# Performance work log

Hardware: AMD Instinct MI355X
Metric: run time of the kernel (lower is better)

The kernel has to match this reference:

```python
import jax, jax.numpy as jnp
from jax import lax
import numpy as np

N, T, PD, TD, F, E, GB = 2048, 256, 5, 5, 128, 65536, 5


def _lstm_layer(x, Wih, Whh, bih, bhh):
    # x: [B, T, D] -> [B, T, H], torch LSTM gate order (i, f, g, o)
    B = x.shape[0]
    H = Whh.shape[1]
    b = bih + bhh

    def step(carry, xt):
        h, c = carry
        gates = xt @ Wih.T + h @ Whh.T + b
        i, f, g, o = jnp.split(gates, 4, axis=-1)
        c = jax.nn.sigmoid(f) * c + jax.nn.sigmoid(i) * jnp.tanh(g)
        h = jax.nn.sigmoid(o) * jnp.tanh(c)
        return (h, c), h

    h0 = jnp.zeros((B, H), x.dtype)
    _, hs = lax.scan(step, (h0, h0), jnp.swapaxes(x, 0, 1))
    return jnp.swapaxes(hs, 0, 1)


def _attention(x, W1, b1, W2, b2):
    # Fused prefix (cumulative causal) softmax attention.
    # Original loops over t computing softmax(scores[:, :t+1]); here:
    # ctx[t] = cumsum(e * x)[t] / cumsum(e)[t] with a global max shift
    # (softmax is shift-invariant, so this equals the per-prefix softmax).
    s = (jnp.tanh(x @ W1.T + b1) @ W2.T + b2)[..., 0]  # [B, T]
    e = jnp.exp(s - jnp.max(s, axis=1, keepdims=True))  # [B, T]
    num = jnp.cumsum(e[..., None] * x, axis=1)          # [B, T, D]
    den = jnp.cumsum(e, axis=1)[..., None]              # [B, T, 1]
    return jnp.sum(num / den, axis=1)                   # [B, D]


def _gcn(x, W, b, edge_index, edge_weight):
    # PyG GCNConv with normalize=True: add self-loops (w=1), symmetric norm.
    n = x.shape[0]
    loop = jnp.arange(n)
    row = jnp.concatenate([edge_index[0], loop])
    col = jnp.concatenate([edge_index[1], loop])
    w = jnp.concatenate([edge_weight, jnp.ones((n,), edge_weight.dtype)])
    deg = jax.ops.segment_sum(w, col, num_segments=n)
    dinv = jnp.where(deg > 0, deg ** -0.5, 0.0)
    norm = dinv[row] * w * dinv[col]
    h = x @ W.T
    out = jax.ops.segment_sum(norm[:, None] * h[row], col, num_segments=n)
    return out + b


def _forward(price, global_trend, p_weights, t_weights,
             lp_Wih0, lp_Whh0, lp_bih0, lp_bhh0, lp_Wih1, lp_Whh1, lp_bih1, lp_bhh1,
             lt_Wih0, lt_Whh0, lt_bih0, lt_bhh0, lt_Wih1, lt_Whh1, lt_bih1, lt_bhh1,
             ap_W1, ap_b1, ap_W2, ap_b2, at_W1, at_b1, at_W2, at_b2,
             gp1_W, gp1_b, gp2_W, gp2_b, gt1_W, gt1_b, gt2_W, gt2_b,
             mlp_W, mlp_b, p_edge_index, t_edge_index):
    x = _lstm_layer(price, lp_Wih0, lp_Whh0, lp_bih0, lp_bhh0)
    x = _lstm_layer(x, lp_Wih1, lp_Whh1, lp_bih1, lp_bhh1)
    x = _attention(x, ap_W1, ap_b1, ap_W2, ap_b2)            # [N, F]
    g = _lstm_layer(global_trend, lt_Wih0, lt_Whh0, lt_bih0, lt_bhh0)
    g = _lstm_layer(g, lt_Wih1, lt_Whh1, lt_bih1, lt_bhh1)
    g = _attention(g, at_W1, at_b1, at_W2, at_b2)            # [GB, F]
    pg = _gcn(x, gp1_W, gp1_b, p_edge_index, p_weights)
    pg = _gcn(pg, gp2_W, gp2_b, p_edge_index, p_weights)     # [N, F]
    # NOTE: original feeds x (not g) into the trend graph convs.
    tg = _gcn(x, gt1_W, gt1_b, t_edge_index, t_weights)
    tg = _gcn(tg, gt2_W, gt2_b, t_edge_index, t_weights)     # [N, F]
    trend = tg @ g.T                                         # [N, GB]
    feat = jnp.concatenate([pg, trend], axis=1)              # [N, F+GB]
    return jax.nn.sigmoid(feat @ mlp_W.T + mlp_b)            # [N, 1]


def setup_inputs() -> dict:
    key = jax.random.key(0)
    ks = iter(jax.random.split(key, 64))
    nrm = lambda shape, s=0.05: jax.random.normal(next(ks), shape, jnp.float32) * s
    inp = {}
    inp['price'] = jax.random.normal(next(ks), (N, T, PD), jnp.float32)
    inp['global_trend'] = jax.random.normal(next(ks), (GB, T, TD), jnp.float32)
    inp['p_edge_index'] = jax.random.randint(next(ks), (2, E), 0, N)
    inp['p_weights'] = jax.random.uniform(next(ks), (E,), jnp.float32)
    inp['t_edge_index'] = jax.random.randint(next(ks), (2, E), 0, N)
    inp['t_weights'] = jax.random.uniform(next(ks), (E,), jnp.float32)
    for pre, d in (('lp', PD), ('lt', TD)):
        inp[pre + '_Wih0'] = nrm((4 * F, d)); inp[pre + '_Whh0'] = nrm((4 * F, F))
        inp[pre + '_bih0'] = nrm((4 * F,));   inp[pre + '_bhh0'] = nrm((4 * F,))
        inp[pre + '_Wih1'] = nrm((4 * F, F)); inp[pre + '_Whh1'] = nrm((4 * F, F))
        inp[pre + '_bih1'] = nrm((4 * F,));   inp[pre + '_bhh1'] = nrm((4 * F,))
    for pre in ('ap', 'at'):
        inp[pre + '_W1'] = nrm((F, F)); inp[pre + '_b1'] = jnp.zeros((F,), jnp.float32)
        inp[pre + '_W2'] = nrm((1, F)); inp[pre + '_b2'] = jnp.zeros((1,), jnp.float32)
    for pre in ('gp', 'gt'):
        inp[pre + '1_W'] = nrm((16, F)); inp[pre + '1_b'] = jnp.zeros((16,), jnp.float32)
        inp[pre + '2_W'] = nrm((F, 16)); inp[pre + '2_b'] = jnp.zeros((F,), jnp.float32)
    inp['mlp_W'] = nrm((1, F + GB)); inp['mlp_b'] = jnp.zeros((1,), jnp.float32)
    return inp


def reference(price, global_trend, p_edge_index, p_weights, t_edge_index, t_weights,
              lp_Wih0, lp_Whh0, lp_bih0, lp_bhh0, lp_Wih1, lp_Whh1, lp_bih1, lp_bhh1,
              lt_Wih0, lt_Whh0, lt_bih0, lt_bhh0, lt_Wih1, lt_Whh1, lt_bih1, lt_bhh1,
              ap_W1, ap_b1, ap_W2, ap_b2, at_W1, at_b1, at_W2, at_b2,
              gp1_W, gp1_b, gp2_W, gp2_b, gt1_W, gt1_b, gt2_W, gt2_b,
              mlp_W, mlp_b):
    return _forward(price, global_trend, p_weights, t_weights,
                    lp_Wih0, lp_Whh0, lp_bih0, lp_bhh0, lp_Wih1, lp_Whh1, lp_bih1, lp_bhh1,
                    lt_Wih0, lt_Whh0, lt_bih0, lt_bhh0, lt_Wih1, lt_Whh1, lt_bih1, lt_bhh1,
                    ap_W1, ap_b1, ap_W2, ap_b2, at_W1, at_b1, at_W2, at_b2,
                    gp1_W, gp1_b, gp2_W, gp2_b, gt1_W, gt1_b, gt2_W, gt2_b,
                    mlp_W, mlp_b, p_edge_index, t_edge_index)
```

## Files before the change

kernel.cpp:

```cpp
#include <hip/hip_runtime.h>
#include <hip/hip_bf16.h>
#include <cstddef>

#define TT    256
#define NROW  2048
#define GBN   5
#define EDG   65536

using f32x4  = __attribute__((ext_vector_type(4))) float;
using bf16x8 = __attribute__((ext_vector_type(8))) short;

__device__ __forceinline__ void pinv(bf16x8& x) { asm volatile("" : "+v"(x)); }

__device__ __forceinline__ void barrier_lgkm() {
  asm volatile("s_waitcnt lgkmcnt(0)" ::: "memory");
  __builtin_amdgcn_s_barrier();
}

__device__ __forceinline__ float exp2fa(float x) { float r; asm("v_exp_f32 %0, %1" : "=v"(r) : "v"(x)); return r; }
__device__ __forceinline__ float rcpfa(float x)  { float r; asm("v_rcp_f32 %0, %1" : "=v"(r) : "v"(x)); return r; }
#define L2E 1.4426950408889634f
__device__ __forceinline__ float sigf(float x) { return rcpfa(1.0f + exp2fa(x * -L2E)); }
__device__ __forceinline__ float tanh_fast(float x) {
  float t = exp2fa(x * (-2.0f * L2E));
  return (1.0f - t) * rcpfa(1.0f + t);
}

enum : int {
  XBUF   = 425984,
  GBUFO  = 688128,
  DINVP  = 688768,
  DINVT  = 690816,
  H16    = 692864,
  PG1    = 725632,
// ... 51 lines not shown
    float x = (k < K1) ? Wa[(size_t)j * K1 + k] : Wb[(size_t)j * K2 + (k - K1)];
    __hip_bfloat16 hi = __float2bfloat16(x);
    ushort u;
    if (part == 0) {
      u = *(ushort*)&hi;
    } else {
      float lo = x - __bfloat162float(hi);
      __hip_bfloat16 lob = __float2bfloat16(lo);
      u = *(ushort*)&lob;
    }
    o[e] = (short)u;
  }
  ((bf16x8*)dst)[t] = o;
}

__global__ void k_zero(float* __restrict__ p, int n) {
  int i = blockIdx.x * blockDim.x + threadIdx.x;
  if (i < n) p[i] = 0.0f;
}
__global__ void k_fill1(float* __restrict__ p, int n) {
  int i = blockIdx.x * blockDim.x + threadIdx.x;
  if (i < n) p[i] = 1.0f;
}
__global__ void k_deg(const int* __restrict__ col, const float* __restrict__ w,
                      float* __restrict__ deg, int n) {
  int i = blockIdx.x * blockDim.x + threadIdx.x;
  if (i < n) atomicAdd(&deg[col[i]], w[i]);
}
__global__ void k_dinv(float* __restrict__ deg, int n) {
  int i = blockIdx.x * blockDim.x + threadIdx.x;
  if (i < n) deg[i] = rsqrtf(deg[i]);
}

__device__ static void lstm0_body(
    SmemPipe* sm, int b,
    const float* __restrict__ price, const float* __restrict__ gtrend,
    const float* __restrict__ ws_ro, ushort* __restrict__ h0W,
    const ushort* __restrict__ h0R, float* __restrict__ c0S,
    const float* __restrict__ Wih0p, const float* __restrict__ bi0p, const float* __restrict__ bh0p,
    const float* __restrict__ Wih0t, const float* __restrict__ bi0t, const float* __restrict__ bh0t,
    int t0, int TCp, int first)
{
  const int tid = threadIdx.x;
  const int w = tid >> 6, l = tid & 63;
  const int lq = l >> 4, lr = l & 15;
  const int rb = lq * 4;
  const int kcol = w * 16 + lr;
  const bool isP = b < 64;
  const int R = isP ? 32 : GBN;
  const float* seq = isP ? (price + (size_t)b * 32 * (TT * 5)) : gtrend;
  const ushort* S0 = (const ushort*)(ws_ro + (isP ? N_P0 : N_T0));
  const float* Wih0 = isP ? Wih0p : Wih0t;
  const float* bi0 = isP ? bi0p : bi0t;
  const float* bh0 = isP ? bh0p : bh0t;

  auto h0hi = sm->a;
  auto h0lo = sm->b;
  float* xsa = sm->x;

  bf16x8 wh[4][4], wl[4][4];
  #pragma unroll
  for (int kk = 0; kk < 4; ++kk)
    #pragma unroll
    for (int g = 0; g < 4; ++g) {
      int blk = (kk * 32 + (w + 8 * g)) * 2;
      wh[kk][g] = ((const bf16x8*)S0)[(blk + 0) * 64 + l];
      wl[kk][g] = ((const bf16x8*)S0)[(blk + 1) * 64 + l];
      pinv(wh[kk][g]); pinv(wl[kk][g]);
    }
  float wih0r[4][5], bg0[4];
  #pragma unroll
  for (int g = 0; g < 4; ++g) {
    int j = kcol + 128 * g;
    bg0[g] = bi0[j] + bh0[j];
    #pragma unroll
    for (int k = 0; k < 5; ++k) wih0r[g][k] = Wih0[j * 5 + k];
  }

  const size_t bstr = (size_t)b * (size_t)TCp * 8192;
  float c0[2][4] = {{0, 0, 0, 0}, {0, 0, 0, 0}};

  for (int i = tid; i < TCp * 160; i += 512) {
    int tl = i / 160, rem = i % 160, r = rem / 5, k = rem % 5;
    xsa[tl * 160 + rem] = (r < R) ? seq[(size_t)r * (TT * 5) + (size_t)(t0 + tl) * 5 + k] : 0.0f;
  }
  if (first) {
    for (int i = tid; i < 4096; i += 512) { h0hi[0][i] = 0; h0lo[0][i] = 0; }
  } else {
    const size_t lb = bstr + (size_t)(TCp - 1) * 8192;
    *(uint4*)&h0hi[0][8 * tid] = *(const uint4*)&h0R[lb + 8 * tid];
    *(uint4*)&h0lo[0][8 * tid] = *(const uint4*)&h0R[lb + 4096 + 8 * tid];
    #pragma unroll
    for (int t = 0; t < 2; ++t)
      #pragma unroll
      for (int reg = 0; reg < 4; ++reg)
        c0[t][reg] = c0S[(size_t)b * 4096 + (size_t)(t * 16 + rb + reg) * 128 + kcol];
  }
  __syncthreads();

  const int kkhi = (kcol >> 3) & 3;
  const int eo = kcol & 7;
  const int b0w = rb + 16 * kkhi;
  const int kkw = kcol >> 5;
  int wro[4];
  #pragma unroll
  for (int reg = 0; reg < 4; ++reg) wro[reg] = kkw * 512 + (b0w + (reg ^ lq)) * 8 + eo;
  const int rdo = (l ^ ((l >> 2) & 3)) * 8;

  int cur = 0;
  for (int tl = 0; tl < TCp; ++tl) {
    const int nxt = cur ^ 1;
    if (tl > 0) {
      *(uint4*)&h0W[bstr + (size_t)(tl - 1) * 8192 + 8 * tid] = *(const uint4*)&h0hi[cur][8 * tid];
      *(uint4*)&h0W[bstr + (size_t)(tl - 1) * 8192 + 4096 + 8 * tid] = *(const uint4*)&h0lo[cur][8 * tid];
    }

    f32x4 acc[2][4];
    #pragma unroll
    for (int t = 0; t < 2; ++t)
      #pragma unroll
      for (int g = 0; g < 4; ++g) acc[t][g] = (f32x4){bg0[g], bg0[g], bg0[g], bg0[g]};
    #pragma unroll
    for (int k = 0; k < 5; ++k) {
      float xv[2][4];
      #pragma unroll
      for (int t = 0; t < 2; ++t)
        #pragma unroll
        for (int reg = 0; reg < 4; ++reg)
          xv[t][reg] = xsa[tl * 160 + (t * 16 + rb + reg) * 5 + k];
      #pragma unroll
      for (int t = 0; t < 2; ++t)
        #pragma unroll
        for (int g = 0; g < 4; ++g)
          #pragma unroll
          for (int reg = 0; reg < 4; ++reg)
            acc[t][g][reg] = fmaf(xv[t][reg], wih0r[g][k], acc[t][g][reg]);
    }
    #pragma unroll
    for (int kk = 0; kk < 4; ++kk) {
      bf16x8 ah0 = *(const bf16x8*)&h0hi[cur][kk * 512 + rdo];
      bf16x8 al0 = *(const bf16x8*)&h0lo[cur][kk * 512 + rdo];
      bf16x8 ah1 = *(const bf16x8*)&h0hi[cur][2048 + kk * 512 + rdo];
      bf16x8 al1 = *(const bf16x8*)&h0lo[cur][2048 + kk * 512 + rdo];
      #pragma unroll
      for (int g = 0; g < 4; ++g) {
        acc[0][g] = __builtin_amdgcn_mfma_f32_16x16x32_bf16(ah0, wh[kk][g], acc[0][g], 0, 0, 0);
        acc[0][g] = __builtin_amdgcn_mfma_f32_16x16x32_bf16(al0, wh[kk][g], acc[0][g], 0, 0, 0);
        acc[0][g] = __builtin_amdgcn_mfma_f32_16x16x32_bf16(ah0, wl[kk][g], acc[0][g], 0, 0, 0);
        acc[1][g] = __builtin_amdgcn_mfma_f32_16x16x32_bf16(ah1, wh[kk][g], acc[1][g], 0, 0, 0);
        acc[1][g] = __builtin_amdgcn_mfma_f32_16x16x32_bf16(al1, wh[kk][g], acc[1][g], 0, 0, 0);
        acc[1][g] = __builtin_amdgcn_mfma_f32_16x16x32_bf16(ah1, wl[kk][g], acc[1][g], 0, 0, 0);
      }
    }
    #pragma unroll
    for (int t = 0; t < 2; ++t)
      #pragma unroll
      for (int reg = 0; reg < 4; ++reg) {
        float gi = acc[t][0][reg], gf = acc[t][1][reg], gg = acc[t][2][reg], go = acc[t][3][reg];
        float c = sigf(gf) * c0[t][reg] + sigf(gi) * tanh_fast(gg);
        c0[t][reg] = c;
        float h = sigf(go) * tanh_fast(c);
        __hip_bfloat16 hb = __float2bfloat16(h);
        float lo = h - __bfloat162float(hb);
        __hip_bfloat16 lb = __float2bfloat16(lo);
        h0hi[nxt][t * 2048 + wro[reg]] = *(ushort*)&hb;
        h0lo[nxt][t * 2048 + wro[reg]] = *(ushort*)&lb;
      }
    barrier_lgkm();
    cur = nxt;
  }
  *(uint4*)&h0W[bstr + (size_t)(TCp - 1) * 8192 + 8 * tid] = *(const uint4*)&h0hi[cur][8 * tid];
  *(uint4*)&h0W[bstr + (size_t)(TCp - 1) * 8192 + 4096 + 8 * tid] = *(const uint4*)&h0lo[cur][8 * tid];

  #pragma unroll
  for (int t = 0; t < 2; ++t)
    #pragma unroll
    for (int reg = 0; reg < 4; ++reg)
      c0S[(size_t)b * 4096 + (size_t)(t * 16 + rb + reg) * 128 + kcol] = c0[t][reg];
}

__device__ static void lstm1_body(
    SmemPipe* sm, int b16,
    const ushort* __restrict__ h0R, float* __restrict__ pre1, const float* __restrict__ ws_ro,
    float* __restrict__ xout, float* __restrict__ gout,
    float* __restrict__ c1S, ushort* __restrict__ h1imgS, float* __restrict__ smS,
    float* __restrict__ numS, float* __restrict__ accOS,
    const float* __restrict__ bi1p, const float* __restrict__ bh1p,
    const float* __restrict__ apB1, const float* __restrict__ apW2, const float* __restrict__ apB2,
    const float* __restrict__ bi1t, const float* __restrict__ bh1t,
    const float* __restrict__ atB1, const float* __restrict__ atW2, const float* __restrict__ atB2,
    int TCp, int first)
{
  const int tid = threadIdx.x;
  const int w = tid >> 6, l = tid & 63;
  const int lq = l >> 4, lr = l & 15;
  const int rb = lq * 4;
  const int kcol = w * 16 + lr;
  const bool isP = b16 < 128;
  const int R = isP ? 16 : GBN;
  const ushort* S1I = (const ushort*)(ws_ro + (isP ? N_P1I : N_T1I));
  const ushort* S1H = (const ushort*)(ws_ro + (isP ? N_P1H : N_T1H));
  const ushort* SA  = (const ushort*)(ws_ro + (isP ? N_PA : N_TA));
  const float* bi1 = isP ? bi1p : bi1t;
  const float* bh1 = isP ? bh1p : bh1t;
  const float* b1ap = isP ? apB1 : atB1;
  const float* w2p  = isP ? apW2 : atW2;
  const float  b2v  = isP ? apB2[0] : atB2[0];

  auto h1hi = sm->a;
  auto h1lo = sm->b;
  auto sbuf = sm->s;

  const int rdo = (l ^ ((l >> 2) & 3)) * 8;
  float* pblk = pre1 + (size_t)b16 * TCp * 8192;

  {
    const int b32 = b16 >> 1, tile = b16 & 1;
    const size_t bstr32 = (size_t)b32 * (size_t)TCp * 8192;
    float bg1[4];
    #pragma unroll
    for (int g = 0; g < 4; ++g) bg1[g] = bi1[kcol + 128 * g] + bh1[kcol + 128 * g];
    for (int g0 = 0; g0 < TCp; g0 += 2) {
      f32x4 pacc[2][4];
      #pragma unroll
      for (int ts = 0; ts < 2; ++ts)
        #pragma unroll
        for (int g = 0; g < 4; ++g) pacc[ts][g] = (f32x4){bg1[g], bg1[g], bg1[g], bg1[g]};
      #pragma unroll
      for (int kk = 0; kk < 4; ++kk) {
        bf16x8 bh_[4], bl_[4];
        #pragma unroll
        for (int g = 0; g < 4; ++g) {
          int blk = (kk * 32 + (w + 8 * g)) * 2;
          bh_[g] = ((const bf16x8*)S1I)[(blk + 0) * 64 + l];
          bl_[g] = ((const bf16x8*)S1I)[(blk + 1) * 64 + l];
        }
        #pragma unroll
        for (int ts = 0; ts < 2; ++ts) {
          const size_t tb = bstr32 + (size_t)(g0 + ts) * 8192 + tile * 2048 + kk * 512 + rdo;
          bf16x8 ah = *(const bf16x8*)&h0R[tb];
          bf16x8 al = *(const bf16x8*)&h0R[tb + 4096];
          #pragma unroll
          for (int g = 0; g < 4; ++g) {
            pacc[ts][g] = __builtin_amdgcn_mfma_f32_16x16x32_bf16(ah, bh_[g], pacc[ts][g], 0, 0, 0);
            pacc[ts][g] = __builtin_amdgcn_mfma_f32_16x16x32_bf16(al, bh_[g], pacc[ts][g], 0, 0, 0);
            pacc[ts][g] = __builtin_amdgcn_mfma_f32_16x16x32_bf16(ah, bl_[g], pacc[ts][g], 0, 0, 0);
          }
        }
      }
      #pragma unroll
      for (int ts = 0; ts < 2; ++ts)
        #pragma unroll
        for (int g = 0; g < 4; ++g)
          *(f32x4*)&pblk[(size_t)(g0 + ts) * 8192 + (size_t)tid * 16 + g * 4] = pacc[ts][g];
    }
    asm volatile("s_waitcnt vmcnt(0)" ::: "memory");
  }

  bf16x8 hh[4][4], hl[4][4];
  #pragma unroll
  for (int kk = 0; kk < 4; ++kk)
    #pragma unroll
    for (int g = 0; g < 4; ++g) {
      int blk = (kk * 32 + (w + 8 * g)) * 2;
      hh[kk][g] = ((const bf16x8*)S1H)[(blk + 0) * 64 + l];
      hl[kk][g] = ((const bf16x8*)S1H)[(blk + 1) * 64 + l];
      pinv(hh[kk][g]); pinv(hl[kk][g]);
    }
  bf16x8 wa[4], wal[4];
  #pragma unroll
  for (int kk = 0; kk < 4; ++kk) {
    wa[kk]  = ((const bf16x8*)SA)[((kk * 8 + w) * 2 + 0) * 64 + l];
    wal[kk] = ((const bf16x8*)SA)[((kk * 8 + w) * 2 + 1) * 64 + l];
    pinv(wa[kk]); pinv(wal[kk]);
  }
  const float w2r = w2p[kcol], b1ar = b1ap[kcol];

  float c1[4] = {0, 0, 0, 0}, h1r[4] = {0, 0, 0, 0}, h1r_prev[4];
  float num[4] = {0, 0, 0, 0}, accO[4] = {0, 0, 0, 0};
  float m_run[4], den_r[4];

  if (first) {
    for (int i = tid; i < 2048; i += 512) { h1hi[0][i] = 0; h1lo[0][i] = 0; }
    #pragma unroll
    for (int reg = 0; reg < 4; ++reg) { m_run[reg] = -1e30f; den_r[reg] = 0.0f; }
  } else {
    const size_t ib = (size_t)b16 * 4096;
    *(uint2*)&h1hi[0][4 * tid] = *(const uint2*)&h1imgS[ib + 4 * tid];
    *(uint2*)&h1lo[0][4 * tid] = *(const uint2*)&h1imgS[ib + 2048 + 4 * tid];
    const size_t sb = (size_t)b16 * 2048;
    #pragma unroll
    for (int reg = 0; reg < 4; ++reg) {
      size_t o = sb + (size_t)(rb + reg) * 128 + kcol;
      c1[reg] = c1S[o];
      num[reg] = numS[o];
      accO[reg] = accOS[o];
      m_run[reg] = smS[(size_t)b16 * 32 + (size_t)(rb + reg) * 2];
      den_r[reg] = smS[(size_t)b16 * 32 + (size_t)(rb + reg) * 2 + 1];
    }
  }
  __syncthreads();

  const int kkhi = (kcol >> 3) & 3;
  const int eo = kcol & 7;
  const int b0w = rb + 16 * kkhi;
  const int kkw = kcol >> 5;
  int wro[4];
  #pragma unroll
  for (int reg = 0; reg < 4; ++reg) wro[reg] = kkw * 512 + (b0w + (reg ^ lq)) * 8 + eo;

  const float* pbase = pblk + (size_t)tid * 16;

  f32x4 pnext[4];
  #pragma unroll
  for (int g = 0; g < 4; ++g) pnext[g] = *(const f32x4*)&pbase[g * 4];

  int cur = 0;
  for (int tl = 0; tl < TCp; ++tl) {
    const int nxt = cur ^ 1;
    f32x4 acc[4];
    #pragma unroll
    for (int g = 0; g < 4; ++g) acc[g] = pnext[g];
    if (tl + 1 < TCp) {
      #pragma unroll
      for (int g = 0; g < 4; ++g)
        pnext[g] = *(const f32x4*)&pbase[(size_t)(tl + 1) * 8192 + g * 4];
    }

    #pragma unroll
    for (int kk = 0; kk < 4; ++kk) {
      bf16x8 ah = *(const bf16x8*)&h1hi[cur][kk * 512 + rdo];
      bf16x8 al = *(const bf16x8*)&h1lo[cur][kk * 512 + rdo];
      #pragma unroll
      for (int g = 0; g < 4; ++g) {
        acc[g] = __builtin_amdgcn_mfma_f32_16x16x32_bf16(ah, hh[kk][g], acc[g], 0, 0, 0);
        acc[g] = __builtin_amdgcn_mfma_f32_16x16x32_bf16(al, hh[kk][g], acc[g], 0, 0, 0);
        acc[g] = __builtin_amdgcn_mfma_f32_16x16x32_bf16(ah, hl[kk][g], acc[g], 0, 0, 0);
      }
    }
    #pragma unroll
    for (int reg = 0; reg < 4; ++reg) {
      h1r_prev[reg] = h1r[reg];
      float gi = acc[0][reg], gf = acc[1][reg], gg = acc[2][reg], go = acc[3][reg];
      float c = sigf(gf) * c1[reg] + sigf(gi) * tanh_fast(gg);
      c1[reg] = c;
      float h = sigf(go) * tanh_fast(c);
      h1r[reg] = h;
      __hip_bfloat16 hb = __float2bfloat16(h);
      float lo = h - __bfloat162float(hb);
      __hip_bfloat16 lb = __float2bfloat16(lo);
      h1hi[nxt][wro[reg]] = *(ushort*)&hb;
      h1lo[nxt][wro[reg]] = *(ushort*)&lb;
    }
    barrier_lgkm();

    if (tl > 0) {
      const int pb = (tl - 1) & 1;
      #pragma unroll
      for (int reg = 0; reg < 4; ++reg) {
        float s = b2v;
        #pragma unroll
        for (int ww = 0; ww < 8; ++ww) s += sbuf[pb][ww][rb + reg];
        float m0 = m_run[reg];
        float nm = fmaxf(m0, s);
        float e = exp2fa((s - nm) * L2E), sc = exp2fa((m0 - nm) * L2E);
        float d = den_r[reg] * sc + e;
        m_run[reg] = nm; den_r[reg] = d;
        num[reg] = num[reg] * sc + e * h1r_prev[reg];
        accO[reg] = fmaf(num[reg], rcpfa(d), accO[reg]);
      }
    }

    f32x4 aa = (f32x4){b1ar, b1ar, b1ar, b1ar};
    #pragma unroll
    for (int kk = 0; kk < 4; ++kk) {
      bf16x8 ah = *(const bf16x8*)&h1hi[nxt][kk * 512 + rdo];
      bf16x8 al = *(const bf16x8*)&h1lo[nxt][kk * 512 + rdo];
      aa = __builtin_amdgcn_mfma_f32_16x16x32_bf16(ah, wa[kk], aa, 0, 0, 0);
      aa = __builtin_amdgcn_mfma_f32_16x16x32_bf16(al, wa[kk], aa, 0, 0, 0);
      aa = __builtin_amdgcn_mfma_f32_16x16x32_bf16(ah, wal[kk], aa, 0, 0, 0);
    }
    float p[4];
    #pragma unroll
    for (int reg = 0; reg < 4; ++reg) p[reg] = tanh_fast(aa[reg]) * w2r;
    #pragma unroll
    for (int m = 1; m < 16; m <<= 1) {
      #pragma unroll
      for (int reg = 0; reg < 4; ++reg) p[reg] += __shfl_xor(p[reg], m);
    }
    if (lr == 0) {
      #pragma unroll
      for (int reg = 0; reg < 4; ++reg) sbuf[tl & 1][w][rb + reg] = p[reg];
    }
    cur = nxt;
  }
  barrier_lgkm();
  {
    const int pb = (TCp - 1) & 1;
    #pragma unroll
    for (int reg = 0; reg < 4; ++reg) {
      float s = b2v;
      #pragma unroll
      for (int ww = 0; ww < 8; ++ww) s += sbuf[pb][ww][rb + reg];
      float m0 = m_run[reg];
      float nm = fmaxf(m0, s);
      float e = exp2fa((s - nm) * L2E), sc = exp2fa((m0 - nm) * L2E);
      float d = den_r[reg] * sc + e;
      m_run[reg] = nm; den_r[reg] = d;
      num[reg] = num[reg] * sc + e * h1r[reg];
      accO[reg] = fmaf(num[reg], rcpfa(d), accO[reg]);
    }
  }

  {
    const size_t ib = (size_t)b16 * 4096;
    *(uint2*)&h1imgS[ib + 4 * tid] = *(const uint2*)&h1hi[cur][4 * tid];
    *(uint2*)&h1imgS[ib + 2048 + 4 * tid] = *(const uint2*)&h1lo[cur][4 * tid];
    const size_t sb = (size_t)b16 * 2048;
    #pragma unroll
    for (int reg = 0; reg < 4; ++reg) {
      size_t o = sb + (size_t)(rb + reg) * 128 + kcol;
      c1S[o] = c1[reg];
      numS[o] = num[reg];
      accOS[o] = accO[reg];
    }
    if (w == 0 && lr == 0) {
      #pragma unroll
      for (int reg = 0; reg < 4; ++reg) {
        smS[(size_t)b16 * 32 + (size_t)(rb + reg) * 2] = m_run[reg];
        smS[(size_t)b16 * 32 + (size_t)(rb + reg) * 2 + 1] = den_r[reg];
      }
    }
  }

  float* dstx = isP ? (xout + (size_t)b16 * 16 * 128) : gout;
  #pragma unroll
  for (int reg = 0; reg < 4; ++reg) {
    int r = rb + reg;
    if (r < R) dstx[(size_t)r * 128 + kcol] = accO[reg];
  }
}

__global__ __launch_bounds__(512, 2) void k_pipe(
    const float* __restrict__ price, const float* __restrict__ gtrend,
    const float* __restrict__ ws_ro, ushort* __restrict__ h0W, const ushort* __restrict__ h0R,
    float* __restrict__ c0S,
    const float* __restrict__ Wih0p, const float* __restrict__ bi0p, const float* __restrict__ bh0p,
    const float* __restrict__ Wih0t, const float* __restrict__ bi0t, const float* __restrict__ bh0t,
    float* __restrict__ pre1,
    float* __restrict__ xout, float* __restrict__ gout,
    float* __restrict__ c1S, ushort* __restrict__ h1imgS, float* __restrict__ smS,
    float* __restrict__ numS, float* __restrict__ accOS,
    const float* __restrict__ bi1p, const float* __restrict__ bh1p,
    const float* __restrict__ apB1, const float* __restrict__ apW2, const float* __restrict__ apB2,
    const float* __restrict__ bi1t, const float* __restrict__ bh1t,
    const float* __restrict__ atB1, const float* __restrict__ atW2, const float* __restrict__ atB2,
    int t0A, int TCp, int firstA, int firstB, int doA, int doB)
{
  __shared__ SmemPipe sm;
  const int bid = blockIdx.x;
  if (bid < 65) {
    if (doA)
      lstm0_body(&sm, bid, price, gtrend, ws_ro, h0W, h0R, c0S,
                 Wih0p, bi0p, bh0p, Wih0t, bi0t, bh0t, t0A, TCp, firstA);
  } else {
    if (doB)
      lstm1_body(&sm, bid - 65, h0R, pre1, ws_ro, xout, gout,
                 c1S, h1imgS, smS, numS, accOS,
                 bi1p, bh1p, apB1, apW2, apB2,
                 bi1t, bh1t, atB1, atW2, atB2, TCp, firstB);
  }
}

__global__ void k_lin(const float* __restrict__ x, const float* __restrict__ W,
                      float* __restrict__ h, int M, int K, int n) {
  int i = blockIdx.x * blockDim.x + threadIdx.x;
  if (i >= n) return;
  int r = i / M, m = i % M;
  const float* xr = x + (size_t)r * K;
  const float* wm = W + (size_t)m * K;
  float a = 0.f;
  for (int k = 0; k < K; ++k) a = fmaf(xr[k], wm[k], a);
  h[i] = a;
}

__global__ void k_scatter(const int* __restrict__ rowi, const int* __restrict__ coli,
                          const float* __restrict__ w, const float* __restrict__ dinv,
                          const float* __restrict__ h, float* __restrict__ outp,
                          int M, long long n) {
  long long i = (long long)blockIdx.x * blockDim.x + threadIdx.x;
  if (i >= n) return;
  int e = (int)(i / M), f = (int)(i % M);
  int rs = rowi[e], cd = coli[e];
  float nrm = dinv[rs] * w[e] * dinv[cd];
  atomicAdd(&outp[(size_t)cd * M + f], nrm * h[(size_t)rs * M + f]);
}

__global__ void k_gcn_fin(float* __restrict__ io, const float* __restrict__ h,
                          const float* __restrict__ dinv, const float* __restrict__ b,
                          int M, int n) {
  int i = blockIdx.x * blockDim.x + threadIdx.x;
  if (i >= n) return;
  int v = i / M, f = i % M;
// ... 75 lines not shown
  const float* mlpb = (const float*)d_in[39];

  float* ws = (float*)d_ws;
  float* outp = (float*)d_out;
  if (ws_size < (size_t)WS_END * sizeof(float)) return;

  int TC = 0;
  for (int cand = 32; cand >= 8; cand >>= 1) {
    unsigned long long need = ((unsigned long long)H0S_O +
                               2ULL * 65 * cand * 4096ULL + 129ULL * cand * 8192ULL) * 4ULL;
    if ((unsigned long long)ws_size >= need) { TC = cand; break; }
  }
  if (TC == 0) return;

  k_pack<<<gdiv(16384), 256, 0, stream>>>(lpWhh0, lpWhh0, 128, 128, 32, 4, (ushort*)(ws + N_P0));
  k_pack<<<gdiv(16384), 256, 0, stream>>>(lpWih1, lpWih1, 128, 128, 32, 4, (ushort*)(ws + N_P1I));
  k_pack<<<gdiv(16384), 256, 0, stream>>>(lpWhh1, lpWhh1, 128, 128, 32, 4, (ushort*)(ws + N_P1H));
  k_pack<<<gdiv(4096),  256, 0, stream>>>(apW1,   apW1,   128, 128,  8, 4, (ushort*)(ws + N_PA));
  k_pack<<<gdiv(16384), 256, 0, stream>>>(ltWhh0, ltWhh0, 128, 128, 32, 4, (ushort*)(ws + N_T0));
  k_pack<<<gdiv(16384), 256, 0, stream>>>(ltWih1, ltWih1, 128, 128, 32, 4, (ushort*)(ws + N_T1I));
  k_pack<<<gdiv(16384), 256, 0, stream>>>(ltWhh1, ltWhh1, 128, 128, 32, 4, (ushort*)(ws + N_T1H));
  k_pack<<<gdiv(4096),  256, 0, stream>>>(atW1,   atW1,   128, 128,  8, 4, (ushort*)(ws + N_TA));

  k_fill1<<<gdiv(NROW), 256, 0, stream>>>(ws + DINVP, NROW);
  k_deg<<<gdiv(EDG), 256, 0, stream>>>(p_ei + EDG, p_w, ws + DINVP, EDG);
  k_dinv<<<gdiv(NROW), 256, 0, stream>>>(ws + DINVP, NROW);
  k_fill1<<<gdiv(NROW), 256, 0, stream>>>(ws + DINVT, NROW);
  k_deg<<<gdiv(EDG), 256, 0, stream>>>(t_ei + EDG, t_w, ws + DINVT, EDG);
  k_dinv<<<gdiv(NROW), 256, 0, stream>>>(ws + DINVT, NROW);

  ushort* h0S0 = (ushort*)(ws + H0S_O);
  ushort* h0S1 = h0S0 + (size_t)65 * TC * 8192;
  float*  pre1 = ws + H0S_O + 2LL * 65 * TC * 4096;
  {
    const int CH = TT / TC;
    for (int c = 0; c < CH; ++c) {
      ushort* hA = (c & 1) ? h0S1 : h0S0;
      ushort* hB = (c & 1) ? h0S0 : h0S1;
      k_pipe<<<194, 512, 0, stream>>>(price, gtrend, ws, hA, hB, ws + C0S_O,
                                      lpWih0, lpBih0, lpBhh0,
                                      ltWih0, ltBih0, ltBhh0,
                                      pre1, ws + XBUF, ws + GBUFO,
                                      ws + C1S_O, (ushort*)(ws + H1IMG_O), ws + SMST_O,
                                      ws + NUMS_O, ws + ACCOS_O,
                                      lpBih1, lpBhh1, apB1, apW2, apB2,
                                      ltBih1, ltBhh1, atB1, atW2, atB2,
                                      c * TC, TC,
                                      c == 0 ? 1 : 0, c == 1 ? 1 : 0,
                                      1, c > 0 ? 1 : 0);
    }
    ushort* hB = ((CH - 1) & 1) ? h0S1 : h0S0;
    k_pipe<<<194, 512, 0, stream>>>(price, gtrend, ws, h0S0, hB, ws + C0S_O,
                                    lpWih0, lpBih0, lpBhh0,
                                    ltWih0, ltBih0, ltBhh0,
                                    pre1, ws + XBUF, ws + GBUFO,
                                    ws + C1S_O, (ushort*)(ws + H1IMG_O), ws + SMST_O,
                                    ws + NUMS_O, ws + ACCOS_O,
                                    lpBih1, lpBhh1, apB1, apW2, apB2,
                                    ltBih1, ltBhh1, atB1, atW2, atB2,
                                    0, TC, 0, CH == 1 ? 1 : 0, 0, 1);
  }

  k_lin<<<gdiv(NROW * 16), 256, 0, stream>>>(ws + XBUF, gp1W, ws + H16, 16, 128, NROW * 16);
  k_zero<<<gdiv(NROW * 16), 256, 0, stream>>>(ws + PG1, NROW * 16);
  k_scatter<<<gdiv((long long)EDG * 16), 256, 0, stream>>>(p_ei, p_ei + EDG, p_w, ws + DINVP,
                                                           ws + H16, ws + PG1, 16, (long long)EDG * 16);
  k_gcn_fin<<<gdiv(NROW * 16), 256, 0, stream>>>(ws + PG1, ws + H16, ws + DINVP, gp1b, 16, NROW * 16);
  k_lin<<<gdiv(NROW * 128), 256, 0, stream>>>(ws + PG1, gp2W, ws + H128, 128, 16, NROW * 128);
// ... 19 lines not shown
```

Baseline: 2.063 ms.

## Replace per-chunk pipeline launches with one persistent cooperative kernel using grid sync

The chunked two-stage LSTM pipeline used to be launched once per time chunk, and every launch reloaded the recurrent weights into registers and moved c/h/softmax state through global memory. It now runs as a single cooperative kernel. Weights and recurrent state stay in registers and LDS across chunks, and chunk handoff between the layer-0 and layer-1 roles is done with grid-wide syncs. If the cooperative launch fails, the code falls back to the old multi-launch path. Grid-sync cost and the occupancy limits needed for co-residency are the tradeoffs.

```diff
diff --git a/kernel.cpp b/kernel.cpp
--- a/kernel.cpp
+++ b/kernel.cpp
@@ -1,5 +1,6 @@
 #include <hip/hip_runtime.h>
 #include <hip/hip_bf16.h>
+#include <hip/hip_cooperative_groups.h>
 #include <cstddef>
 
 #define TT    256
@@ -117,89 +118,32 @@
   if (i < n) deg[i] = rsqrtf(deg[i]);
 }
 
-__device__ static void lstm0_body(
-    SmemPipe* sm, int b,
-    const float* __restrict__ price, const float* __restrict__ gtrend,
-    const float* __restrict__ ws_ro, ushort* __restrict__ h0W,
-    const ushort* __restrict__ h0R, float* __restrict__ c0S,
-    const float* __restrict__ Wih0p, const float* __restrict__ bi0p, const float* __restrict__ bh0p,
-    const float* __restrict__ Wih0t, const float* __restrict__ bi0t, const float* __restrict__ bh0t,
-    int t0, int TCp, int first)
+
+__device__ __forceinline__ void roleA_chunk(
+    SmemPipe* sm, int b, int& cur, float (&c0)[2][4],
+    const bf16x8 (&wh)[4][4], const bf16x8 (&wl)[4][4],
+    const float (&wih0r)[4][5], const float (&bg0)[4],
+    const float* __restrict__ seq, int R,
+    ushort* __restrict__ h0W, int t0, int TCp,
+    int tid, int rb, const int (&wro)[4], int rdo)
 {
-  const int tid = threadIdx.x;
-  const int w = tid >> 6, l = tid & 63;
-  const int lq = l >> 4, lr = l & 15;
-  const int rb = lq * 4;
-  const int kcol = w * 16 + lr;
-  const bool isP = b < 64;
-  const int R = isP ? 32 : GBN;
-  const float* seq = isP ? (price + (size_t)b * 32 * (TT * 5)) : gtrend;
-  const ushort* S0 = (const ushort*)(ws_ro + (isP ? N_P0 : N_T0));
-  const float* Wih0 = isP ? Wih0p : Wih0t;
-  const float* bi0 = isP ? bi0p : bi0t;
-  const float* bh0 = isP ? bh0p : bh0t;
-
   auto h0hi = sm->a;
   auto h0lo = sm->b;
   float* xsa = sm->x;
-
-  bf16x8 wh[4][4], wl[4][4];
-  #pragma unroll
-  for (int kk = 0; kk < 4; ++kk)
-    #pragma unroll
-    for (int g = 0; g < 4; ++g) {
-      int blk = (kk * 32 + (w + 8 * g)) * 2;
-      wh[kk][g] = ((const bf16x8*)S0)[(blk + 0) * 64 + l];
-      wl[kk][g] = ((const bf16x8*)S0)[(blk + 1) * 64 + l];
-      pinv(wh[kk][g]); pinv(wl[kk][g]);
-    }
-  float wih0r[4][5], bg0[4];
-  #pragma unroll
-  for (int g = 0; g < 4; ++g) {
-    int j = kcol + 128 * g;
-    bg0[g] = bi0[j] + bh0[j];
-    #pragma unroll
-    for (int k = 0; k < 5; ++k) wih0r[g][k] = Wih0[j * 5 + k];
-  }
-
   const size_t bstr = (size_t)b * (size_t)TCp * 8192;
-  float c0[2][4] = {{0, 0, 0, 0}, {0, 0, 0, 0}};
 
   for (int i = tid; i < TCp * 160; i += 512) {
     int tl = i / 160, rem = i % 160, r = rem / 5, k = rem % 5;
     xsa[tl * 160 + rem] = (r < R) ? seq[(size_t)r * (TT * 5) + (size_t)(t0 + tl) * 5 + k] : 0.0f;
   }
-  if (first) {
-    for (int i = tid; i < 4096; i += 512) { h0hi[0][i] = 0; h0lo[0][i] = 0; }
-  } else {
-    const size_t lb = bstr + (size_t)(TCp - 1) * 8192;
-    *(uint4*)&h0hi[0][8 * tid] = *(const uint4*)&h0R[lb + 8 * tid];
-    *(uint4*)&h0lo[0][8 * tid] = *(const uint4*)&h0R[lb + 4096 + 8 * tid];
-    #pragma unroll
-    for (int t = 0; t < 2; ++t)
-      #pragma unroll
-      for (int reg = 0; reg < 4; ++reg)
-        c0[t][reg] = c0S[(size_t)b * 4096 + (size_t)(t * 16 + rb + reg) * 128 + kcol];
-  }
   __syncthreads();
 
-  const int kkhi = (kcol >> 3) & 3;
-  const int eo = kcol & 7;
-  const int b0w = rb + 16 * kkhi;
-  const int kkw = kcol >> 5;
-  int wro[4];
-  #pragma unroll
-  for (int reg = 0; reg < 4; ++reg) wro[reg] = kkw * 512 + (b0w + (reg ^ lq)) * 8 + eo;
-  const int rdo = (l ^ ((l >> 2) & 3)) * 8;
-
-  int cur = 0;
   for (int tl = 0; tl < TCp; ++tl) {
     const int nxt = cur ^ 1;
     if (tl > 0) {
       *(uint4*)&h0W[bstr + (size_t)(tl - 1) * 8192 + 8 * tid] = *(const uint4*)&h0hi[cur][8 * tid];
       *(uint4*)&h0W[bstr + (size_t)(tl - 1) * 8192 + 4096 + 8 * tid] = *(const uint4*)&h0lo[cur][8 * tid];
     }
-
     f32x4 acc[2][4];
     #pragma unroll
     for (int t = 0; t < 2; ++t)
@@ -256,55 +200,26 @@
   }
   *(uint4*)&h0W[bstr + (size_t)(TCp - 1) * 8192 + 8 * tid] = *(const uint4*)&h0hi[cur][8 * tid];
   *(uint4*)&h0W[bstr + (size_t)(TCp - 1) * 8192 + 4096 + 8 * tid] = *(const uint4*)&h0lo[cur][8 * tid];
-
-  #pragma unroll
-  for (int t = 0; t < 2; ++t)
-    #pragma unroll
-    for (int reg = 0; reg < 4; ++reg)
-      c0S[(size_t)b * 4096 + (size_t)(t * 16 + rb + reg) * 128 + kcol] = c0[t][reg];
-}
-
-__device__ static void lstm1_body(
-    SmemPipe* sm, int b16,
-    const ushort* __restrict__ h0R, float* __restrict__ pre1, const float* __restrict__ ws_ro,
-    float* __restrict__ xout, float* __restrict__ gout,
-    float* __restrict__ c1S, ushort* __restrict__ h1imgS, float* __restrict__ smS,
-    float* __restrict__ numS, float* __restrict__ accOS,
-    const float* __restrict__ bi1p, const float* __restrict__ bh1p,
-    const float* __restrict__ apB1, const float* __restrict__ apW2, const float* __restrict__ apB2,
-    const float* __restrict__ bi1t, const float* __restrict__ bh1t,
-    const float* __restrict__ atB1, const float* __restrict__ atW2, const float* __restrict__ atB2,
-    int TCp, int first)
+}
+
+__device__ __forceinline__ void roleB_chunk(
+    SmemPipe* sm, int b16, int& cur,
+    float (&c1)[4], float (&h1r)[4], float (&num)[4], float (&accO)[4],
+    float (&m_run)[4], float (&den_r)[4],
+    const bf16x8 (&hh)[4][4], const bf16x8 (&hl)[4][4],
+    const bf16x8 (&wa)[4], const bf16x8 (&wal)[4],
+    float w2r, float b1ar, float b2v, const float (&bg1)[4],
+    const ushort* __restrict__ S1I,
+    const ushort* __restrict__ h0R, float* __restrict__ pblk,
+    int TCp, int tid, int w, int l, int rb, const int (&wro)[4], int rdo)
 {
-  const int tid = threadIdx.x;
-  const int w = tid >> 6, l = tid & 63;
-  const int lq = l >> 4, lr = l & 15;
-  const int rb = lq * 4;
-  const int kcol = w * 16 + lr;
-  const bool isP = b16 < 128;
-  const int R = isP ? 16 : GBN;
-  const ushort* S1I = (const ushort*)(ws_ro + (isP ? N_P1I : N_T1I));
-  const ushort* S1H = (const ushort*)(ws_ro + (isP ? N_P1H : N_T1H));
-  const ushort* SA  = (const ushort*)(ws_ro + (isP ? N_PA : N_TA));
-  const float* bi1 = isP ? bi1p : bi1t;
-  const float* bh1 = isP ? bh1p : bh1t;
-  const float* b1ap = isP ? apB1 : atB1;
-  const float* w2p  = isP ? apW2 : atW2;
-  const float  b2v  = isP ? apB2[0] : atB2[0];
-
   auto h1hi = sm->a;
   auto h1lo = sm->b;
   auto sbuf = sm->s;
 
-  const int rdo = (l ^ ((l >> 2) & 3)) * 8;
-  float* pblk = pre1 + (size_t)b16 * TCp * 8192;
-
   {
     const int b32 = b16 >> 1, tile = b16 & 1;
     const size_t bstr32 = (size_t)b32 * (size_t)TCp * 8192;
-    float bg1[4];
-    #pragma unroll
-    for (int g = 0; g < 4; ++g) bg1[g] = bi1[kcol + 128 * g] + bh1[kcol + 128 * g];
     for (int g0 = 0; g0 < TCp; g0 += 2) {
       f32x4 pacc[2][4];
       #pragma unroll
@@ -342,65 +257,12 @@
     asm volatile("s_waitcnt vmcnt(0)" ::: "memory");
   }
 
-  bf16x8 hh[4][4], hl[4][4];
-  #pragma unroll
-  for (int kk = 0; kk < 4; ++kk)
-    #pragma unroll
-    for (int g = 0; g < 4; ++g) {
-      int blk = (kk * 32 + (w + 8 * g)) * 2;
-      hh[kk][g] = ((const bf16x8*)S1H)[(blk + 0) * 64 + l];
-      hl[kk][g] = ((const bf16x8*)S1H)[(blk + 1) * 64 + l];
-      pinv(hh[kk][g]); pinv(hl[kk][g]);
-    }
-  bf16x8 wa[4], wal[4];
-  #pragma unroll
-  for (int kk = 0; kk < 4; ++kk) {
-    wa[kk]  = ((const bf16x8*)SA)[((kk * 8 + w) * 2 + 0) * 64 + l];
-    wal[kk] = ((const bf16x8*)SA)[((kk * 8 + w) * 2 + 1) * 64 + l];
-    pinv(wa[kk]); pinv(wal[kk]);
-  }
-  const float w2r = w2p[kcol], b1ar = b1ap[kcol];
-
-  float c1[4] = {0, 0, 0, 0}, h1r[4] = {0, 0, 0, 0}, h1r_prev[4];
-  float num[4] = {0, 0, 0, 0}, accO[4] = {0, 0, 0, 0};
-  float m_run[4], den_r[4];
-
-  if (first) {
-    for (int i = tid; i < 2048; i += 512) { h1hi[0][i] = 0; h1lo[0][i] = 0; }
-    #pragma unroll
-    for (int reg = 0; reg < 4; ++reg) { m_run[reg] = -1e30f; den_r[reg] = 0.0f; }
-  } else {
-    const size_t ib = (size_t)b16 * 4096;
-    *(uint2*)&h1hi[0][4 * tid] = *(const uint2*)&h1imgS[ib + 4 * tid];
-    *(uint2*)&h1lo[0][4 * tid] = *(const uint2*)&h1imgS[ib + 2048 + 4 * tid];
-    const size_t sb = (size_t)b16 * 2048;
-    #pragma unroll
-    for (int reg = 0; reg < 4; ++reg) {
-      size_t o = sb + (size_t)(rb + reg) * 128 + kcol;
-      c1[reg] = c1S[o];
-      num[reg] = numS[o];
-      accO[reg] = accOS[o];
-      m_run[reg] = smS[(size_t)b16 * 32 + (size_t)(rb + reg) * 2];
-      den_r[reg] = smS[(size_t)b16 * 32 + (size_t)(rb + reg) * 2 + 1];
-    }
-  }
-  __syncthreads();
-
-  const int kkhi = (kcol >> 3) & 3;
-  const int eo = kcol & 7;
-  const int b0w = rb + 16 * kkhi;
-  const int kkw = kcol >> 5;
-  int wro[4];
-  #pragma unroll
-  for (int reg = 0; reg < 4; ++reg) wro[reg] = kkw * 512 + (b0w + (reg ^ lq)) * 8 + eo;
-
   const float* pbase = pblk + (size_t)tid * 16;
-
+  float h1r_prev[4];
   f32x4 pnext[4];
   #pragma unroll
   for (int g = 0; g < 4; ++g) pnext[g] = *(const f32x4*)&pbase[g * 4];
 
-  int cur = 0;
   for (int tl = 0; tl < TCp; ++tl) {
     const int nxt = cur ^ 1;
     f32x4 acc[4];
@@ -411,7 +273,6 @@
       for (int g = 0; g < 4; ++g)
         pnext[g] = *(const f32x4*)&pbase[(size_t)(tl + 1) * 8192 + g * 4];
     }
-
     #pragma unroll
     for (int kk = 0; kk < 4; ++kk) {
       bf16x8 ah = *(const bf16x8*)&h1hi[cur][kk * 512 + rdo];
@@ -473,7 +334,7 @@
       #pragma unroll
       for (int reg = 0; reg < 4; ++reg) p[reg] += __shfl_xor(p[reg], m);
     }
-    if (lr == 0) {
+    if ((l & 15) == 0) {
       #pragma unroll
       for (int reg = 0; reg < 4; ++reg) sbuf[tl & 1][w][rb + reg] = p[reg];
     }
@@ -496,33 +357,137 @@
       accO[reg] = fmaf(num[reg], rcpfa(d), accO[reg]);
     }
   }
-
-  {
-    const size_t ib = (size_t)b16 * 4096;
-    *(uint2*)&h1imgS[ib + 4 * tid] = *(const uint2*)&h1hi[cur][4 * tid];
-    *(uint2*)&h1imgS[ib + 2048 + 4 * tid] = *(const uint2*)&h1lo[cur][4 * tid];
-    const size_t sb = (size_t)b16 * 2048;
+}
+
+struct CoopP {
+  const float *price, *gtrend, *ws_ro;
+  ushort *h0S0, *h0S1;
+  float *pre1, *xout, *gout;
+  const float *Wih0p, *bi0p, *bh0p, *Wih0t, *bi0t, *bh0t;
+  const float *bi1p, *bh1p, *apB1, *apW2, *apB2;
+  const float *bi1t, *bh1t, *atB1, *atW2, *atB2;
+  int TCp, CH;
+};
+
+__global__ __launch_bounds__(512, 2) void k_coop(CoopP P) {
+  namespace cg = cooperative_groups;
+  cg::grid_group gg = cg::this_grid();
+  __shared__ SmemPipe sm;
+  const int bid = blockIdx.x;
+  const int tid = threadIdx.x;
+  const int w = tid >> 6, l = tid & 63;
+  const int lq = l >> 4, lr = l & 15;
+  const int rb = lq * 4;
+  const int kcol = w * 16 + lr;
+  const int rdo = (l ^ ((l >> 2) & 3)) * 8;
+  const int kkhi = (kcol >> 3) & 3;
+  const int eo = kcol & 7;
+  const int b0w = rb + 16 * kkhi;
+  const int kkw = kcol >> 5;
+  int wro[4];
+  #pragma unroll
+  for (int reg = 0; reg < 4; ++reg) wro[reg] = kkw * 512 + (b0w + (reg ^ lq)) * 8 + eo;
+  const int TCp = P.TCp, CH = P.CH;
+
+  if (bid < 65) {
+    const int b = bid;
+    const bool isP = b < 64;
+    const int R = isP ? 32 : GBN;
+    const float* seq = isP ? (P.price + (size_t)b * 32 * (TT * 5)) : P.gtrend;
+    const ushort* S0 = (const ushort*)(P.ws_ro + (isP ? N_P0 : N_T0));
+    const float* Wih0 = isP ? P.Wih0p : P.Wih0t;
+    const float* bi0 = isP ? P.bi0p : P.bi0t;
+    const float* bh0 = isP ? P.bh0p : P.bh0t;
+
+    bf16x8 wh[4][4], wl[4][4];
+    #pragma unroll
+    for (int kk = 0; kk < 4; ++kk)
+      #pragma unroll
+      for (int g = 0; g < 4; ++g) {
+        int blk = (kk * 32 + (w + 8 * g)) * 2;
+        wh[kk][g] = ((const bf16x8*)S0)[(blk + 0) * 64 + l];
+        wl[kk][g] = ((const bf16x8*)S0)[(blk + 1) * 64 + l];
+        pinv(wh[kk][g]); pinv(wl[kk][g]);
+      }
+    float wih0r[4][5], bg0[4];
+    #pragma unroll
+    for (int g = 0; g < 4; ++g) {
+      int j = kcol + 128 * g;
+      bg0[g] = bi0[j] + bh0[j];
+      #pragma unroll
+      for (int k = 0; k < 5; ++k) wih0r[g][k] = Wih0[j * 5 + k];
+    }
+    for (int i = tid; i < 4096; i += 512) { sm.a[0][i] = 0; sm.b[0][i] = 0; }
+    __syncthreads();
+    float c0[2][4] = {{0, 0, 0, 0}, {0, 0, 0, 0}};
+    int cur = 0;
+    for (int it = 0; it <= CH; ++it) {
+      if (it > 0) gg.sync();
+      if (it >= CH) continue;
+      ushort* h0W = (it & 1) ? P.h0S1 : P.h0S0;
+      roleA_chunk(&sm, b, cur, c0, wh, wl, wih0r, bg0, seq, R,
+                  h0W, it * TCp, TCp, tid, rb, wro, rdo);
+    }
+  } else {
+    const int b16 = bid - 65;
+    const bool isP = b16 < 128;
+    const int R = isP ? 16 : GBN;
+    const ushort* S1I = (const ushort*)(P.ws_ro + (isP ? N_P1I : N_T1I));
+    const ushort* S1H = (const ushort*)(P.ws_ro + (isP ? N_P1H : N_T1H));
+    const ushort* SA  = (const ushort*)(P.ws_ro + (isP ? N_PA : N_TA));
+    const float* bi1 = isP ? P.bi1p : P.bi1t;
+    const float* bh1 = isP ? P.bh1p : P.bh1t;
+    const float* b1ap = isP ? P.apB1 : P.atB1;
+    const float* w2p  = isP ? P.apW2 : P.atW2;
+    const float  b2v  = isP ? P.apB2[0] : P.atB2[0];
+
+    bf16x8 hh[4][4], hl[4][4];
+    #pragma unroll
+    for (int kk = 0; kk < 4; ++kk)
+      #pragma unroll
+      for (int g = 0; g < 4; ++g) {
+        int blk = (kk * 32 + (w + 8 * g)) * 2;
+        hh[kk][g] = ((const bf16x8*)S1H)[(blk + 0) * 64 + l];
+        hl[kk][g] = ((const bf16x8*)S1H)[(blk + 1) * 64 + l];
+        pinv(hh[kk][g]); pinv(hl[kk][g]);
+      }
+    bf16x8 wa[4], wal[4];
+    #pragma unroll
+    for (int kk = 0; kk < 4; ++kk) {
+      wa[kk]  = ((const bf16x8*)SA)[((kk * 8 + w) * 2 + 0) * 64 + l];
+      wal[kk] = ((const bf16x8*)SA)[((kk * 8 + w) * 2 + 1) * 64 + l];
+      pinv(wa[kk]); pinv(wal[kk]);
+    }
+    const float w2r = w2p[kcol], b1ar = b1ap[kcol];
+    float bg1[4];
+    #pragma unroll
+    for (int g = 0; g < 4; ++g) bg1[g] = bi1[kcol + 128 * g] + bh1[kcol + 128 * g];
+
+    for (int i = tid; i < 2048; i += 512) { sm.a[0][i] = 0; sm.b[0][i] = 0; }
+    __syncthreads();
+    float c1[4] = {0, 0, 0, 0}, h1r[4] = {0, 0, 0, 0};
+    float num[4] = {0, 0, 0, 0}, accO[4] = {0, 0, 0, 0};
+    float m_run[4], den_r[4];
+    #pragma unroll
+    for (int reg = 0; reg < 4; ++reg) { m_run[reg] = -1e30f; den_r[reg] = 0.0f; }
+    int cur = 0;
+    float* pblk = P.pre1 + (size_t)b16 * TCp * 8192;
+
+    for (int it = 0; it <= CH; ++it) {
+      if (it > 0) gg.sync();
+      if (it == 0) continue;
+      const int c = it - 1;
+      const ushort* h0R = (c & 1) ? P.h0S1 : P.h0S0;
+      roleB_chunk(&sm, b16, cur, c1, h1r, num, accO, m_run, den_r,
+                  hh, hl, wa, wal, w2r, b1ar, b2v, bg1, S1I,
+                  h0R, pblk, TCp, tid, w, l, rb, wro, rdo);
+    }
+    float* dstx = isP ? (P.xout + (size_t)b16 * 16 * 128) : P.gout;
     #pragma unroll
     for (int reg = 0; reg < 4; ++reg) {
-      size_t o = sb + (size_t)(rb + reg) * 128 + kcol;
-      c1S[o] = c1[reg];
-      numS[o] = num[reg];
-      accOS[o] = accO[reg];
-    }
-    if (w == 0 && lr == 0) {
-      #pragma unroll
-      for (int reg = 0; reg < 4; ++reg) {
-        smS[(size_t)b16 * 32 + (size_t)(rb + reg) * 2] = m_run[reg];
-        smS[(size_t)b16 * 32 + (size_t)(rb + reg) * 2 + 1] = den_r[reg];
-      }
-    }
-  }
-
-  float* dstx = isP ? (xout + (size_t)b16 * 16 * 128) : gout;
-  #pragma unroll
-  for (int reg = 0; reg < 4; ++reg) {
-    int r = rb + reg;
-    if (r < R) dstx[(size_t)r * 128 + kcol] = accO[reg];
+      int r = rb + reg;
+      if (r < R) dstx[(size_t)r * 128 + kcol] = accO[reg];
+    }
   }
 }
 
@@ -544,16 +509,159 @@
 {
   __shared__ SmemPipe sm;
   const int bid = blockIdx.x;
+  const int tid = threadIdx.x;
+  const int w = tid >> 6, l = tid & 63;
+  const int lq = l >> 4, lr = l & 15;
+  const int rb = lq * 4;
+  const int kcol = w * 16 + lr;
+  const int rdo = (l ^ ((l >> 2) & 3)) * 8;
+  const int kkhi = (kcol >> 3) & 3;
+  const int eo = kcol & 7;
+  const int b0w = rb + 16 * kkhi;
+  const int kkw = kcol >> 5;
+  int wro[4];
+  #pragma unroll
+  for (int reg = 0; reg < 4; ++reg) wro[reg] = kkw * 512 + (b0w + (reg ^ lq)) * 8 + eo;
+
   if (bid < 65) {
-    if (doA)
-      lstm0_body(&sm, bid, price, gtrend, ws_ro, h0W, h0R, c0S,
-                 Wih0p, bi0p, bh0p, Wih0t, bi0t, bh0t, t0A, TCp, firstA);
+    if (!doA) return;
+    const int b = bid;
+    const bool isP = b < 64;
+    const int R = isP ? 32 : GBN;
+    const float* seq = isP ? (price + (size_t)b * 32 * (TT * 5)) : gtrend;
+    const ushort* S0 = (const ushort*)(ws_ro + (isP ? N_P0 : N_T0));
+    const float* Wih0 = isP ? Wih0p : Wih0t;
+    const float* bi0 = isP ? bi0p : bi0t;
+    const float* bh0 = isP ? bh0p : bh0t;
+    bf16x8 wh[4][4], wl[4][4];
+    #pragma unroll
+    for (int kk = 0; kk < 4; ++kk)
+      #pragma unroll
+      for (int g = 0; g < 4; ++g) {
+        int blk = (kk * 32 + (w + 8 * g)) * 2;
+        wh[kk][g] = ((const bf16x8*)S0)[(blk + 0) * 64 + l];
+        wl[kk][g] = ((const bf16x8*)S0)[(blk + 1) * 64 + l];
+        pinv(wh[kk][g]); pinv(wl[kk][g]);
+      }
+    float wih0r[4][5], bg0[4];
+    #pragma unroll
+    for (int g = 0; g < 4; ++g) {
+      int j = kcol + 128 * g;
+      bg0[g] = bi0[j] + bh0[j];
+      #pragma unroll
+      for (int k = 0; k < 5; ++k) wih0r[g][k] = Wih0[j * 5 + k];
+    }
+    const size_t bstr = (size_t)b * (size_t)TCp * 8192;
+    float c0[2][4] = {{0, 0, 0, 0}, {0, 0, 0, 0}};
+    if (firstA) {
+      for (int i = tid; i < 4096; i += 512) { sm.a[0][i] = 0; sm.b[0][i] = 0; }
+    } else {
+      const size_t lb = bstr + (size_t)(TCp - 1) * 8192;
+      *(uint4*)&sm.a[0][8 * tid] = *(const uint4*)&h0R[lb + 8 * tid];
+      *(uint4*)&sm.b[0][8 * tid] = *(const uint4*)&h0R[lb + 4096 + 8 * tid];
+      #pragma unroll
+      for (int t = 0; t < 2; ++t)
+        #pragma unroll
+        for (int reg = 0; reg < 4; ++reg)
+          c0[t][reg] = c0S[(size_t)b * 4096 + (size_t)(t * 16 + rb + reg) * 128 + kcol];
+    }
+    __syncthreads();
+    int cur = 0;
+    roleA_chunk(&sm, b, cur, c0, wh, wl, wih0r, bg0, seq, R, h0W, t0A, TCp, tid, rb, wro, rdo);
+    #pragma unroll
+    for (int t = 0; t < 2; ++t)
+      #pragma unroll
+      for (int reg = 0; reg < 4; ++reg)
+        c0S[(size_t)b * 4096 + (size_t)(t * 16 + rb + reg) * 128 + kcol] = c0[t][reg];
   } else {
-    if (doB)
-      lstm1_body(&sm, bid - 65, h0R, pre1, ws_ro, xout, gout,
-                 c1S, h1imgS, smS, numS, accOS,
-                 bi1p, bh1p, apB1, apW2, apB2,
-                 bi1t, bh1t, atB1, atW2, atB2, TCp, firstB);
+    if (!doB) return;
+    const int b16 = bid - 65;
+    const bool isP = b16 < 128;
+    const int R = isP ? 16 : GBN;
+    const ushort* S1I = (const ushort*)(ws_ro + (isP ? N_P1I : N_T1I));
+    const ushort* S1H = (const ushort*)(ws_ro + (isP ? N_P1H : N_T1H));
+    const ushort* SA  = (const ushort*)(ws_ro + (isP ? N_PA : N_TA));
+    const float* bi1 = isP ? bi1p : bi1t;
+    const float* bh1 = isP ? bh1p : bh1t;
+    const float* b1ap = isP ? apB1 : atB1;
+    const float* w2p  = isP ? apW2 : atW2;
+    const float  b2v  = isP ? apB2[0] : atB2[0];
+    bf16x8 hh[4][4], hl[4][4];
+    #pragma unroll
+    for (int kk = 0; kk < 4; ++kk)
+      #pragma unroll
+      for (int g = 0; g < 4; ++g) {
+        int blk = (kk * 32 + (w + 8 * g)) * 2;
+        hh[kk][g] = ((const bf16x8*)S1H)[(blk + 0) * 64 + l];
+        hl[kk][g] = ((const bf16x8*)S1H)[(blk + 1) * 64 + l];
+        pinv(hh[kk][g]); pinv(hl[kk][g]);
+      }
+    bf16x8 wa[4], wal[4];
+    #pragma unroll
+    for (int kk = 0; kk < 4; ++kk) {
+      wa[kk]  = ((const bf16x8*)SA)[((kk * 8 + w) * 2 + 0) * 64 + l];
+      wal[kk] = ((const bf16x8*)SA)[((kk * 8 + w) * 2 + 1) * 64 + l];
+      pinv(wa[kk]); pinv(wal[kk]);
+    }
+    const float w2r = w2p[kcol], b1ar = b1ap[kcol];
+    float bg1[4];
+    #pragma unroll
+    for (int g = 0; g < 4; ++g) bg1[g] = bi1[kcol + 128 * g] + bh1[kcol + 128 * g];
+
+    float c1[4] = {0, 0, 0, 0}, h1r[4] = {0, 0, 0, 0};
+    float num[4] = {0, 0, 0, 0}, accO[4] = {0, 0, 0, 0};
+    float m_run[4], den_r[4];
+    if (firstB) {
+      for (int i = tid; i < 2048; i += 512) { sm.a[0][i] = 0; sm.b[0][i] = 0; }
+      #pragma unroll
+      for (int reg = 0; reg < 4; ++reg) { m_run[reg] = -1e30f; den_r[reg] = 0.0f; }
+    } else {
+      const size_t ib = (size_t)b16 * 4096;
+      *(uint2*)&sm.a[0][4 * tid] = *(const uint2*)&h1imgS[ib + 4 * tid];
+      *(uint2*)&sm.b[0][4 * tid] = *(const uint2*)&h1imgS[ib + 2048 + 4 * tid];
+      const size_t sb = (size_t)b16 * 2048;
+      #pragma unroll
+      for (int reg = 0; reg < 4; ++reg) {
+        size_t o = sb + (size_t)(rb + reg) * 128 + kcol;
+        c1[reg] = c1S[o];
+        num[reg] = numS[o];
+        accO[reg] = accOS[o];
+        m_run[reg] = smS[(size_t)b16 * 32 + (size_t)(rb + reg) * 2];
+        den_r[reg] = smS[(size_t)b16 * 32 + (size_t)(rb + reg) * 2 + 1];
+      }
+    }
+    __syncthreads();
+    int cur = 0;
+    float* pblk = pre1 + (size_t)b16 * TCp * 8192;
+    roleB_chunk(&sm, b16, cur, c1, h1r, num, accO, m_run, den_r,
+                hh, hl, wa, wal, w2r, b1ar, b2v, bg1, S1I,
+                h0R, pblk, TCp, tid, w, l, rb, wro, rdo);
+    {
+      const size_t ib = (size_t)b16 * 4096;
+      *(uint2*)&h1imgS[ib + 4 * tid] = *(const uint2*)&sm.a[cur][4 * tid];
+      *(uint2*)&h1imgS[ib + 2048 + 4 * tid] = *(const uint2*)&sm.b[cur][4 * tid];
+      const size_t sb = (size_t)b16 * 2048;
+      #pragma unroll
+      for (int reg = 0; reg < 4; ++reg) {
+        size_t o = sb + (size_t)(rb + reg) * 128 + kcol;
+        c1S[o] = c1[reg];
+        numS[o] = num[reg];
+        accOS[o] = accO[reg];
+      }
+      if (w == 0 && (l & 15) == 0) {
+        #pragma unroll
+        for (int reg = 0; reg < 4; ++reg) {
+          smS[(size_t)b16 * 32 + (size_t)(rb + reg) * 2] = m_run[reg];
+          smS[(size_t)b16 * 32 + (size_t)(rb + reg) * 2 + 1] = den_r[reg];
+        }
+      }
+    }
+    float* dstx = isP ? (xout + (size_t)b16 * 16 * 128) : gout;
+    #pragma unroll
+    for (int reg = 0; reg < 4; ++reg) {
+      int r = rb + reg;
+      if (r < R) dstx[(size_t)r * 128 + kcol] = accO[reg];
+    }
   }
 }
 
@@ -695,8 +803,26 @@
   ushort* h0S0 = (ushort*)(ws + H0S_O);
   ushort* h0S1 = h0S0 + (size_t)65 * TC * 8192;
   float*  pre1 = ws + H0S_O + 2LL * 65 * TC * 4096;
+  const int CH = TT / TC;
+
+  bool coop_ok = false;
   {
-    const int CH = TT / TC;
+    CoopP P;
+    P.price = price; P.gtrend = gtrend; P.ws_ro = ws;
+    P.h0S0 = h0S0; P.h0S1 = h0S1; P.pre1 = pre1;
+    P.xout = ws + XBUF; P.gout = ws + GBUFO;
+    P.Wih0p = lpWih0; P.bi0p = lpBih0; P.bh0p = lpBhh0;
+    P.Wih0t = ltWih0; P.bi0t = ltBih0; P.bh0t = ltBhh0;
+    P.bi1p = lpBih1; P.bh1p = lpBhh1; P.apB1 = apB1; P.apW2 = apW2; P.apB2 = apB2;
+    P.bi1t = ltBih1; P.bh1t = ltBhh1; P.atB1 = atB1; P.atW2 = atW2; P.atB2 = atB2;
+    P.TCp = TC; P.CH = CH;
+    void* args[] = {(void*)&P};
+    hipError_t e = hipLaunchCooperativeKernel((const void*)k_coop, dim3(194), dim3(512),
+                                              args, 0, stream);
+    if (e == hipSuccess) coop_ok = true;
+    else (void)hipGetLastError();
+  }
+  if (!coop_ok) {
     for (int c = 0; c < CH; ++c) {
       ushort* hA = (c & 1) ? h0S1 : h0S0;
       ushort* hB = (c & 1) ? h0S0 : h0S1;
```

Result: slower. 2.395 ms (+16.1%).
